# Performance work log

Measured on AMD Instinct MI355X. Metric: run time of the kernel, lower is better.

## Reference

```python
import jax, jax.numpy as jnp
import numpy as np
from jax import lax

K_DIM, E_DIM, H_DIM, BETA = 256, 64, 256, 0.25
DN = ('NCHW', 'OIHW', 'NCHW')


def conv(x, w, b=None, stride=1, pad=0):
    y = lax.conv_general_dilated(x, w, (stride, stride), [(pad, pad), (pad, pad)], dimension_numbers=DN)
    if b is not None:
        y = y + b[None, :, None, None]
    return y


def deconv(x, w, b):
    # torch ConvTranspose2d(k=4, stride=2, pad=1): weight [in, out, kH, kW]
    rhs = jnp.flip(w, (2, 3)).swapaxes(0, 1)  # -> [out, in, kH, kW]
    y = lax.conv_general_dilated(x, rhs, (1, 1), [(2, 2), (2, 2)], lhs_dilation=(2, 2), dimension_numbers=DN)
    return y + b[None, :, None, None]


def res_block(x, w3, w1):
    out = jax.nn.relu(x)
    out = conv(out, w3, stride=1, pad=1)
    out = jax.nn.relu(out)
    out = conv(out, w1, stride=1, pad=0)
    return out + x


def vq_embed(z, codebook):
    # z: [B, C, Hs, Ws]; faithful to original: flatten to (-1, e_dim) even though C != e_dim
    zp = jnp.transpose(z, (0, 2, 3, 1))  # [B,Hs,Ws,C]
    zf = zp.reshape(-1, E_DIM)  # [N, e_dim]
    # ||z||^2 + ||e||^2 - 2 z e^T
    dist = (jnp.sum(zf * zf, axis=1, keepdims=True)
            + jnp.sum(codebook * codebook, axis=1)
            - 2.0 * zf @ codebook.T)  # [N, K]
    idx = jnp.argmin(dist, axis=1)  # [N]
    vq = jnp.take(codebook, idx, axis=0).reshape(zp.shape)  # gather == one-hot matmul
    loss = (jnp.mean((lax.stop_gradient(vq) - zp) ** 2)
            + BETA * jnp.mean((vq - lax.stop_gradient(zp)) ** 2))
    vq_st = zp + lax.stop_gradient(vq - zp)  # straight-through
    return loss, jnp.transpose(vq_st, (0, 3, 1, 2))


def setup_inputs() -> dict:
    key = jax.random.key(0)
    ks = jax.random.split(key, 20)
    f32 = jnp.float32
    s = 0.05
    inp = {
        'x': jax.random.normal(ks[0], (32, 3, 128, 128), f32),
        'enc_w1': jax.random.normal(ks[1], (H_DIM, 3, 4, 4), f32) * s,
        'enc_b1': jnp.zeros((H_DIM,), f32),
        'enc_w2': jax.random.normal(ks[2], (H_DIM, H_DIM, 4, 4), f32) * s,
        'enc_b2': jnp.zeros((H_DIM,), f32),
        'er1_w3': jax.random.normal(ks[3], (H_DIM, H_DIM, 3, 3), f32) * s,
        'er1_w1': jax.random.normal(ks[4], (H_DIM, H_DIM, 1, 1), f32) * s,
        'er2_w3': jax.random.normal(ks[5], (H_DIM, H_DIM, 3, 3), f32) * s,
        'er2_w1': jax.random.normal(ks[6], (H_DIM, H_DIM, 1, 1), f32) * s,
        'codebook': jax.random.uniform(ks[7], (K_DIM, E_DIM), f32, -1.0 / K_DIM, 1.0 / K_DIM),
        'dr1_w3': jax.random.normal(ks[8], (H_DIM, H_DIM, 3, 3), f32) * s,
        'dr1_w1': jax.random.normal(ks[9], (H_DIM, H_DIM, 1, 1), f32) * s,
        'dr2_w3': jax.random.normal(ks[10], (H_DIM, H_DIM, 3, 3), f32) * s,
        'dr2_w1': jax.random.normal(ks[11], (H_DIM, H_DIM, 1, 1), f32) * s,
        'dt1_w': jax.random.normal(ks[12], (H_DIM, H_DIM, 4, 4), f32) * s,  # [in,out,k,k]
        'dt1_b': jnp.zeros((H_DIM,), f32),
        'dt2_w': jax.random.normal(ks[13], (H_DIM, 3, 4, 4), f32) * s,
        'dt2_b': jnp.zeros((3,), f32),
    }
    return inp


def reference(x, enc_w1, enc_b1, enc_w2, enc_b2, er1_w3, er1_w1, er2_w3, er2_w1,
              codebook, dr1_w3, dr1_w1, dr2_w3, dr2_w1, dt1_w, dt1_b, dt2_w, dt2_b):
    # encoder
    z = conv(x, enc_w1, enc_b1, stride=2, pad=1)
    z = conv(z, enc_w2, enc_b2, stride=2, pad=1)
    z = res_block(z, er1_w3, er1_w1)
    z = res_block(z, er2_w3, er2_w1)
    # VQ
    emb_loss, vq_z = vq_embed(z, codebook)
    # decoder
    d = res_block(vq_z, dr1_w3, dr1_w1)
    d = res_block(d, dr2_w3, dr2_w1)
    d = deconv(d, dt1_w, dt1_b)
    d = deconv(d, dt2_w, dt2_b)
    recon = jnp.tanh(d)
    return recon, emb_loss
```

## Files before the change

kernel.cpp:

```cpp
#include <hip/hip_runtime.h>
#include <math.h>


typedef unsigned short ushort;
typedef short bf16x8 __attribute__((ext_vector_type(8)));
typedef float f32x4 __attribute__((ext_vector_type(4)));

__device__ __forceinline__ ushort f2bf(float f) {
    unsigned u = __builtin_bit_cast(unsigned, f);
    unsigned r = (u + 0x7fffu + ((u >> 16) & 1u)) >> 16;
    return (ushort)r;
}
__device__ __forceinline__ float bfl(unsigned u) { return __builtin_bit_cast(float, u << 16); }
__device__ __forceinline__ float bfh(unsigned u) { return __builtin_bit_cast(float, u & 0xffff0000u); }

__device__ __forceinline__ unsigned relu_u(unsigned u) {
    unsigned m = (u >> 15) & 0x00010001u;
    return u & ~((m << 16) - m);
}
__device__ __forceinline__ uint4 relu4(uint4 v) {
    v.x = relu_u(v.x); v.y = relu_u(v.y); v.z = relu_u(v.z); v.w = relu_u(v.w);
    return v;
}

__global__ void k_pack_c3x4(const float* __restrict__ w0, const float* __restrict__ w1,
                            const float* __restrict__ w2, const float* __restrict__ w3,
                            ushort* __restrict__ o0, ushort* __restrict__ o1,
                            ushort* __restrict__ o2, ushort* __restrict__ o3) {
    int layer = blockIdx.x / 2304;
    int i = (blockIdx.x - layer * 2304) * 256 + threadIdx.x;
    const float* w = layer == 0 ? w0 : layer == 1 ? w1 : layer == 2 ? w2 : w3;
    ushort* o = layer == 0 ? o0 : layer == 1 ? o1 : layer == 2 ? o2 : o3;
    int kk = i & 31, co = (i >> 5) & 255, cb = (i >> 13) & 7, t = i >> 16;
    int ci = cb * 32 + kk, kh = t / 3, kw = t % 3;
    o[i] = f2bf(w[((co * 256 + ci) * 3 + kh) * 3 + kw]);
}

__global__ void k_pack_c1x1x4(const float* __restrict__ w0, const float* __restrict__ w1,
                              const float* __restrict__ w2, const float* __restrict__ w3,
                              ushort* __restrict__ o0, ushort* __restrict__ o1,
                              ushort* __restrict__ o2, ushort* __restrict__ o3) {
    int layer = blockIdx.x >> 8;
    int i = (blockIdx.x & 255) * 256 + threadIdx.x;
    const float* w = layer == 0 ? w0 : layer == 1 ? w1 : layer == 2 ? w2 : w3;
    ushort* o = layer == 0 ? o0 : layer == 1 ? o1 : layer == 2 ? o2 : o3;
    int kk = i & 31, co = (i >> 5) & 255, cb = (i >> 13) & 7;
    o[i] = f2bf(w[co * 256 + cb * 32 + kk]);
}

__global__ void k_pack_vq(const float* __restrict__ cb, ushort* __restrict__ apk,
                          float* __restrict__ en) {
    if (blockIdx.x < 64) {
        int i = blockIdx.x * 256 + threadIdx.x;
        int j = i & 7, lane = (i >> 3) & 63, s = (i >> 9) & 1, t = i >> 10;
        int code = t * 16 + (lane & 15);
        int dim = s * 32 + (lane >> 4) * 8 + j;
        apk[i] = f2bf(cb[code * 64 + dim]);
    } else {
        int code = threadIdx.x;
        float s = 0.f;
        for (int d = 0; d < 64; ++d) { float v = cb[code * 64 + d]; s += v * v; }
        en[code] = s;
    }
}

__global__ __launch_bounds__(256) void k_wcomp_enc(const float* __restrict__ w1,
                                                   const float* __restrict__ b1f,
                                                   const float* __restrict__ w2,
                                                   const float* __restrict__ b2f,
                                                   ushort* __restrict__ wenc,
                                                   float* __restrict__ benc,
                                                   float* __restrict__ wct,
                                                   float* __restrict__ wcb,
                                                   float* __restrict__ wcl,
                                                   float* __restrict__ wcr,
                                                   float* __restrict__ wcc) {
    __shared__ float sw1[12288];
    __shared__ float sw2[4096];
    __shared__ float part[2400];
    int co = blockIdx.x, tid = threadIdx.x;
    for (int i = tid; i < 12288; i += 256) sw1[i] = w1[i];
    for (int i = tid; i < 4096; i += 256) sw2[i] = w2[co * 4096 + i];
    __syncthreads();

    {
        float s = 0.f;
#pragma unroll
        for (int t = 0; t < 16; ++t) s += sw2[tid * 16 + t];
        float pb = b1f[tid] * s;
#pragma unroll
        for (int m = 1; m < 64; m <<= 1) pb += __shfl_xor(pb, m);
        if ((tid & 63) == 0) part[tid >> 6] = pb;
    }
    __syncthreads();
    if (tid == 0) benc[co] = b2f[co] + part[0] + part[1] + part[2] + part[3];

    if (tid < 240) {
        int y = tid / 24, rem = tid % 24, ci = rem / 8, ms = rem % 8;
        int na = 0, aa[2], h1[2];
#pragma unroll
        for (int a = 0; a < 4; ++a) {
            int k1 = y - 2 * a;
            if ((unsigned)k1 < 4u) { aa[na] = a; h1[na] = k1; ++na; }
        }
        float acc10[10];
#pragma unroll
        for (int xx = 0; xx < 10; ++xx) acc10[xx] = 0.f;
        for (int m = ms * 32; m < ms * 32 + 32; ++m) {
            for (int pa = 0; pa < na; ++pa) {
                float4 a2 = *(const float4*)&sw2[m * 16 + aa[pa] * 4];
                float4 a1 = *(const float4*)&sw1[m * 48 + ci * 16 + h1[pa] * 4];
                acc10[0] += a2.x * a1.x; acc10[1] += a2.x * a1.y; acc10[2] += a2.x * a1.z; acc10[3] += a2.x * a1.w;
                acc10[2] += a2.y * a1.x; acc10[3] += a2.y * a1.y; acc10[4] += a2.y * a1.z; acc10[5] += a2.y * a1.w;
                acc10[4] += a2.z * a1.x; acc10[5] += a2.z * a1.y; acc10[6] += a2.z * a1.z; acc10[7] += a2.z * a1.w;
                acc10[6] += a2.w * a1.x; acc10[7] += a2.w * a1.y; acc10[8] += a2.w * a1.z; acc10[9] += a2.w * a1.w;
            }
        }
#pragma unroll
        for (int xx = 0; xx < 10; ++xx) part[tid * 10 + xx] = acc10[xx];
    }
    __syncthreads();
    for (int w = tid; w < 320; w += 256) {
        if (w < 300) {
            int y = w / 30, r = w % 30, ci = r / 10, xx = r % 10;
            float s = 0.f;
#pragma unroll
            for (int ms = 0; ms < 8; ++ms) s += part[((y * 24 + ci * 8) + ms) * 10 + xx];
            wenc[(y * 256 + co) * 32 + xx * 3 + ci] = f2bf(s);
        } else {
            int j = w - 300;
            int y = j >> 1;
            wenc[(y * 256 + co) * 32 + 30 + (j & 1)] = 0;
        }
    }

    if (tid < 30 || (tid >= 32 && tid < 62)) {
        bool top = tid < 30;
        int t = top ? tid : tid - 32;
        int xx = t / 3, ci = t % 3;
        int k2hf = top ? 0 : 3, k1hf = top ? 3 : 0;
        float s = 0.f;
        for (int m = 0; m < 256; ++m)
            for (int k2w = 0; k2w < 4; ++k2w) {
                int k1w = xx - 2 * k2w;
                if ((unsigned)k1w < 4u)
                    s += sw2[m * 16 + k2hf * 4 + k2w] * sw1[m * 48 + ci * 16 + k1hf * 4 + k1w];
            }
        (top ? wct : wcb)[t * 256 + co] = s;
    } else if ((tid >= 64 && tid < 94) || (tid >= 96 && tid < 126)) {
        bool left = tid < 94;
        int t = left ? tid - 64 : tid - 96;
        int y = t / 3, ci = t % 3;
        int k2wf = left ? 0 : 3, k1wf = left ? 3 : 0;
        float s = 0.f;
        for (int m = 0; m < 256; ++m)
            for (int k2h = 0; k2h < 4; ++k2h) {
                int k1h = y - 2 * k2h;
                if ((unsigned)k1h < 4u)
                    s += sw2[m * 16 + k2h * 4 + k2wf] * sw1[m * 48 + ci * 16 + k1h * 4 + k1wf];
            }
        (left ? wcl : wcr)[t * 256 + co] = s;
    } else if (tid >= 128 && tid < 140) {
        int c = (tid - 128) / 3, ci = (tid - 128) % 3;
        int k2h = (c >> 1) ? 3 : 0, k2w = (c & 1) ? 3 : 0;
        int k1h = 3 - k2h, k1w = 3 - k2w;
        float s = 0.f;
        for (int m = 0; m < 256; ++m)
            s += sw2[m * 16 + k2h * 4 + k2w] * sw1[m * 48 + ci * 16 + k1h * 4 + k1w];
        wcc[(c * 3 + ci) * 256 + co] = s;
    }
}

__global__ __launch_bounds__(256) void k_wcomp_dec(const float* __restrict__ dt1,
                                                   const float* __restrict__ dt1b,
                                                   const float* __restrict__ dt2,
                                                   const float* __restrict__ dt2b,
                                                   ushort* __restrict__ wdec,
                                                   float* __restrict__ bdec) {
    __shared__ float s1[4096];
    __shared__ float s2[12288];
    __shared__ float part[2400];
    int ci = blockIdx.x, tid = threadIdx.x;
    for (int i = tid; i < 4096; i += 256) s1[i] = dt1[ci * 4096 + i];
    for (int i = tid; i < 12288; i += 256) s2[i] = dt2[i];
    __syncthreads();

    if (ci == 0 && tid < 48) {
        int o = tid >> 4, p = tid & 15, py = p >> 2, px = p & 3;
        int c0 = (py + 1) & 1, d0 = (px + 1) & 1;
        float s = dt2b[o];
        for (int m = 0; m < 256; ++m) {
            float t2 = s2[m * 48 + o * 16 + c0 * 4 + d0] + s2[m * 48 + o * 16 + c0 * 4 + d0 + 2]
                     + s2[m * 48 + o * 16 + (c0 + 2) * 4 + d0] + s2[m * 48 + o * 16 + (c0 + 2) * 4 + d0 + 2];
            s += dt1b[m] * t2;
        }
        bdec[tid] = s;
    }

    if (tid < 240) {
        int y = tid / 24, rem = tid % 24, o = rem / 8, ms = rem % 8;
        int na = 0, aa[2], cc[2];
#pragma unroll
        for (int a = 0; a < 4; ++a) {
            int c = y - 2 * a;
            if ((unsigned)c < 4u) { aa[na] = a; cc[na] = c; ++na; }
        }
        float acc10[10];
#pragma unroll
        for (int xx = 0; xx < 10; ++xx) acc10[xx] = 0.f;
        for (int m = ms * 32; m < ms * 32 + 32; ++m) {
            for (int pa = 0; pa < na; ++pa) {
                float4 d1 = *(const float4*)&s1[m * 16 + aa[pa] * 4];
                float4 d2 = *(const float4*)&s2[m * 48 + o * 16 + cc[pa] * 4];
                acc10[0] += d1.x * d2.x; acc10[1] += d1.x * d2.y; acc10[2] += d1.x * d2.z; acc10[3] += d1.x * d2.w;
                acc10[2] += d1.y * d2.x; acc10[3] += d1.y * d2.y; acc10[4] += d1.y * d2.z; acc10[5] += d1.y * d2.w;
                acc10[4] += d1.z * d2.x; acc10[5] += d1.z * d2.y; acc10[6] += d1.z * d2.z; acc10[7] += d1.z * d2.w;
                acc10[6] += d1.w * d2.x; acc10[7] += d1.w * d2.y; acc10[8] += d1.w * d2.z; acc10[9] += d1.w * d2.w;
            }
        }
#pragma unroll
        for (int xx = 0; xx < 10; ++xx) part[tid * 10 + xx] = acc10[xx];
    }
    __syncthreads();
    for (int w = tid; w < 300; w += 256) {
        int y = w / 30, r = w % 30, o = r / 10, xx = r % 10;
        float s = 0.f;
#pragma unroll
        for (int ms = 0; ms < 8; ++ms) s += part[((y * 24 + o * 8) + ms) * 10 + xx];
        int du = (y < 3) ? 1 : (y < 7) ? 0 : -1;
        int py = y - 3 + 4 * du;
        int dv = (xx < 3) ? 1 : (xx < 7) ? 0 : -1;
        int px = xx - 3 + 4 * dv;
        int t = (du + 1) * 3 + (dv + 1);
        int cb2 = ci >> 5, kk = ci & 31;
        wdec[((((t * 3 + o) * 8 + cb2) * 16 + py * 4 + px) * 32) + kk] = f2bf(s);
    }
}

__global__ void k_xpack(const float* __restrict__ x, ushort* __restrict__ xpk) {
    int i = blockIdx.x * 256 + threadIdx.x;
    int k = i & 31, ow = (i >> 5) & 31, r = (i >> 10) & 127, n = i >> 17;
    float v = 0.f;
    if (k < 30) {
        int ci = k % 3, kw = k / 3;
        int col = 4 * ow - 3 + kw;
        if ((unsigned)col < 128u) v = x[((n * 3 + ci) * 128 + r) * 128 + col];
    }
    xpk[i] = f2bf(v);
}

__global__ __launch_bounds__(128) void k_enc_comp(const ushort* __restrict__ xpk,
                                                  const ushort* __restrict__ wenc,
                                                  const float* __restrict__ benc,
                                                  ushort* __restrict__ obf) {
    int tid = threadIdx.x, lane = tid & 63, wv = tid >> 6;
    int q = lane >> 4, l15 = lane & 15;
    int b = blockIdx.x;
    int mblk = b & 7, coslab = (b >> 3) & 3, n = b >> 5;
    int R0 = mblk * 4 + wv * 2;
    int aoff = (coslab * 64 + l15) * 32 + q * 8;

    f32x4 acc[4][4];
#pragma unroll
    for (int at = 0; at < 4; ++at)
#pragma unroll
        for (int bt = 0; bt < 4; ++bt) acc[at][bt] = 0.f;

    for (int t = 0; t < 10; ++t) {
        bf16x8 af[4];
#pragma unroll
        for (int at = 0; at < 4; ++at)
            af[at] = *(const bf16x8*)(wenc + t * 8192 + aoff + at * 512);
#pragma unroll
        for (int bt2 = 0; bt2 < 2; ++bt2) {
            int irow = 4 * (R0 + bt2) + t - 3;
            if ((unsigned)irow >= 128u) continue;
            bf16x8 bf[2];
#pragma unroll
            for (int hb = 0; hb < 2; ++hb) {
                int ow = hb * 16 + l15;
                bf[hb] = *(const bf16x8*)(xpk + (((long)n * 128 + irow) * 32 + ow) * 32 + q * 8);
            }
#pragma unroll
            for (int at = 0; at < 4; ++at)
#pragma unroll
                for (int hb = 0; hb < 2; ++hb)
                    acc[at][bt2 * 2 + hb] = __builtin_amdgcn_mfma_f32_16x16x32_bf16(
                        af[at], bf[hb], acc[at][bt2 * 2 + hb], 0, 0, 0);
        }
    }

    int co_base = coslab * 64;
#pragma unroll
    for (int at = 0; at < 4; ++at) {
        int co_t = co_base + at * 16 + q * 4;
        float4 b4 = *(const float4*)(benc + co_t);
        float bv[4] = {b4.x, b4.y, b4.z, b4.w};
#pragma unroll
        for (int bt = 0; bt < 4; ++bt) {
            int m = R0 * 32 + bt * 16 + l15;
            long oaddr = ((long)n * 1024 + m) * 256 + co_t;
            float v[4];
#pragma unroll
            for (int r = 0; r < 4; ++r) v[r] = acc[at][bt][r] + bv[r];
            uint2 pk;
            pk.x = (unsigned)f2bf(v[0]) | ((unsigned)f2bf(v[1]) << 16);
            pk.y = (unsigned)f2bf(v[2]) | ((unsigned)f2bf(v[3]) << 16);
            *(uint2*)(obf + oaddr) = pk;
        }
    }
}

__global__ __launch_bounds__(256) void k_fix_border(const float* __restrict__ x,
                                                    const ushort* __restrict__ xpk,
                                                    const float* __restrict__ wct,
                                                    const float* __restrict__ wcb,
                                                    const float* __restrict__ wcl,
                                                    const float* __restrict__ wcr,
                                                    const float* __restrict__ wcc,
                                                    ushort* __restrict__ X0) {
    int b = blockIdx.x;
    int n = b >> 7, job = b & 127;
    if (job >= 124) return;
    int co = threadIdx.x;

    auto dot_tb = [&](const float* __restrict__ w, int row, int qq) -> float {
        const ushort* xr = xpk + (((long)n * 128 + row) * 32 + qq) * 32;
        float s = 0.f;
        for (int k = 0; k < 30; ++k) s += w[k * 256 + co] * bfl((unsigned)xr[k]);
        return s;
    };
    auto dot_lr = [&](const float* __restrict__ w, int p, int colofs) -> float {
        float s = 0.f;
        for (int y = 0; y < 10; ++y) {
            int row = 4 * p - 3 + y;
            if ((unsigned)row >= 128u) continue;
            for (int ci = 0; ci < 3; ++ci)
                s += w[(y * 3 + ci) * 256 + co] * x[((long)(n * 3 + ci) * 128 + row) * 128 + colofs];
        }
        return s;
    };
    auto corner = [&](int c, int row, int colofs) -> float {
        float s = 0.f;
        for (int ci = 0; ci < 3; ++ci)
            s += wcc[(c * 3 + ci) * 256 + co] * x[((long)(n * 3 + ci) * 128 + row) * 128 + colofs];
        return s;
    };

    int m;
    float corr;
    if (job < 32) {
        int qq = job;
        m = qq;
        corr = dot_tb(wct, 0, qq);
        if (qq == 0)  corr += dot_lr(wcl, 0, 0)   - corner(0, 0, 0);
        if (qq == 31) corr += dot_lr(wcr, 0, 127) - corner(1, 0, 127);
    } else if (job < 64) {
        int qq = job - 32;
        m = 992 + qq;
        corr = dot_tb(wcb, 127, qq);
        if (qq == 0)  corr += dot_lr(wcl, 31, 0)   - corner(2, 127, 0);
        if (qq == 31) corr += dot_lr(wcr, 31, 127) - corner(3, 127, 127);
    } else if (job < 94) {
        int p = job - 63;
        m = 32 * p;
        corr = dot_lr(wcl, p, 0);
    } else {
        int p = job - 93;
        m = 32 * p + 31;
        corr = dot_lr(wcr, p, 127);
    }

    ushort* ptr = X0 + ((long)n * 1024 + m) * 256 + co;
    float v = bfl((unsigned)(*ptr));
    *ptr = f2bf(v - corr);
}

__global__ __launch_bounds__(256, 2) void k_resblock(const ushort* __restrict__ xin,
                                                     const ushort* __restrict__ w3pk,
                                                     const ushort* __restrict__ w1pk,
                                                     ushort* __restrict__ obf) {
    constexpr int BUFU = 4 * 4 * 34 * 8;
    __shared__ __align__(16) ushort sX[2 * BUFU];
    __shared__ __align__(16) ushort sEx[64 * 256];

    int tid = threadIdx.x, lane = tid & 63, wv = tid >> 6;
    int q = lane >> 4, l15 = lane & 15;
    int b = blockIdx.x;
    int rp = b & 15, n = b >> 4;
    int R0 = rp * 2;

    if (tid < 64) {
        int bufi = tid >> 5, rq = (tid >> 1) & 15, cc = (tid & 1) ? 33 : 0;
        uint4 z; z.x = z.y = z.z = z.w = 0;
        *(uint4*)&sX[bufi * BUFU + (rq * 34 + cc) * 8] = z;
    }

    int brr[4], bcol[4];
#pragma unroll
    for (int bt = 0; bt < 4; ++bt) {
        int p = bt * 16 + l15;
        brr[bt] = p >> 5; bcol[bt] = (p & 31) + 1;
    }

    int scol = lane >> 1, j0 = (lane & 1) * 2;
    int aoff = (wv * 64 + l15) * 32 + q * 8;

    f32x4 acc[4][4];
#pragma unroll
    for (int at = 0; at < 4; ++at)
#pragma unroll
        for (int bt = 0; bt < 4; ++bt) acc[at][bt] = 0.f;

    int hh = R0 - 1 + wv;
    bool hvalid = (unsigned)hh < 32u;
    uint4 sreg[2];
    auto stage_load = [&](int cb2) {
        long off = (((long)n * 32 + hh) * 32 + scol) * 256 + cb2 * 32 + j0 * 8;
#pragma unroll
        for (int k = 0; k < 2; ++k) {
            uint4 v;
            if (hvalid) v = relu4(*(const uint4*)(xin + off + k * 8));
            else { v.x = 0; v.y = 0; v.z = 0; v.w = 0; }
            sreg[k] = v;
        }
    };
    auto write_stage = [&](int pbuf) {
        ushort* bufp = sX + pbuf * BUFU;
#pragma unroll
        for (int k = 0; k < 2; ++k)
            *(uint4*)&bufp[((wv * 4 + j0 + k) * 34 + scol + 1) * 8] = sreg[k];
    };

    stage_load(0);
    write_stage(0);
    __syncthreads();

    for (int cb = 0; cb < 8; ++cb) {
        ushort* bufp = sX + (cb & 1) * BUFU;
        if (cb + 1 < 8) stage_load(cb + 1);
        const ushort* wb = w3pk + (long)cb * 8192 + aoff;

        bf16x8 afc[4];
#pragma unroll
        for (int at = 0; at < 4; ++at) afc[at] = *(const bf16x8*)(wb + at * 512);
#pragma unroll
        for (int t = 0; t < 9; ++t) {
            bf16x8 afn[4];
            if (t < 8) {
#pragma unroll
                for (int at = 0; at < 4; ++at)
                    afn[at] = *(const bf16x8*)(wb + (long)(t + 1) * 65536 + at * 512);
            }
            int taprow = t / 3, dx = t % 3 - 1;
            bf16x8 bfr[4];
#pragma unroll
            for (int bt = 0; bt < 4; ++bt)
                bfr[bt] = *(const bf16x8*)&bufp[(((brr[bt] + taprow) * 4 + q) * 34 + bcol[bt] + dx) * 8];
#pragma unroll
            for (int at = 0; at < 4; ++at)
#pragma unroll
                for (int bt = 0; bt < 4; ++bt)
                    acc[at][bt] = __builtin_amdgcn_mfma_f32_16x16x32_bf16(afc[at], bfr[bt],
                                                                          acc[at][bt], 0, 0, 0);
            if (t < 8) {
#pragma unroll
                for (int at = 0; at < 4; ++at) afc[at] = afn[at];
            }
        }

        if (cb + 1 < 8) {
            write_stage((cb + 1) & 1);
            __syncthreads();
        }
    }

#pragma unroll
    for (int at = 0; at < 4; ++at) {
        int co_t = wv * 64 + at * 16 + q * 4;
#pragma unroll
        for (int bt = 0; bt < 4; ++bt) {
            int px = bt * 16 + l15;
            uint2 pk;
            pk.x = (unsigned)f2bf(fmaxf(acc[at][bt][0], 0.f))
                 | ((unsigned)f2bf(fmaxf(acc[at][bt][1], 0.f)) << 16);
            pk.y = (unsigned)f2bf(fmaxf(acc[at][bt][2], 0.f))
                 | ((unsigned)f2bf(fmaxf(acc[at][bt][3], 0.f)) << 16);
            *(uint2*)&sEx[px * 256 + (co_t ^ ((px & 7) << 3))] = pk;
        }
    }
    __syncthreads();

    f32x4 acc2[4][4];
#pragma unroll
    for (int at = 0; at < 4; ++at)
#pragma unroll
        for (int bt = 0; bt < 4; ++bt) acc2[at][bt] = 0.f;

    for (int cb = 0; cb < 8; ++cb) {
        const ushort* wb1 = w1pk + (long)cb * 8192 + aoff;
        bf16x8 af1[4];
#pragma unroll
        for (int at = 0; at < 4; ++at) af1[at] = *(const bf16x8*)(wb1 + at * 512);
        bf16x8 bf1[4];
#pragma unroll
        for (int bt = 0; bt < 4; ++bt) {
            int px = bt * 16 + l15;
            bf1[bt] = *(const bf16x8*)&sEx[px * 256 + ((cb * 32 + q * 8) ^ ((px & 7) << 3))];
        }
#pragma unroll
        for (int at = 0; at < 4; ++at)
#pragma unroll
            for (int bt = 0; bt < 4; ++bt)
                acc2[at][bt] = __builtin_amdgcn_mfma_f32_16x16x32_bf16(af1[at], bf1[bt],
                                                                      acc2[at][bt], 0, 0, 0);
    }

#pragma unroll
    for (int at = 0; at < 4; ++at) {
        int co_t = wv * 64 + at * 16 + q * 4;
#pragma unroll
        for (int bt = 0; bt < 4; ++bt) {
            int m = R0 * 32 + bt * 16 + l15;
            long oaddr = ((long)n * 1024 + m) * 256 + co_t;
            uint2 rr = *(const uint2*)(xin + oaddr);
            float v[4];
            v[0] = acc2[at][bt][0] + bfl(rr.x);
            v[1] = acc2[at][bt][1] + bfh(rr.x);
            v[2] = acc2[at][bt][2] + bfl(rr.y);
            v[3] = acc2[at][bt][3] + bfh(rr.y);
            uint2 pk;
            pk.x = (unsigned)f2bf(v[0]) | ((unsigned)f2bf(v[1]) << 16);
            pk.y = (unsigned)f2bf(v[2]) | ((unsigned)f2bf(v[3]) << 16);
            *(uint2*)(obf + oaddr) = pk;
        }
    }
}

__global__ __launch_bounds__(256) void k_vq2(const ushort* __restrict__ zb,
                                             const ushort* __restrict__ apk,
                                             const float* __restrict__ en,
                                             const float* __restrict__ cbf,
                                             ushort* __restrict__ vqb,
                                             float* __restrict__ loss) {
    __shared__ int sIdx[64];
    __shared__ float sLoss[64];
    int tid = threadIdx.x, lane = tid & 63, wv = tid >> 6;
    int q = lane >> 4, l15 = lane & 15;
    int r0 = blockIdx.x * 64;
    int R = r0 + wv * 16;

    const ushort* zp = zb + ((long)(R + l15)) * 64 + q * 8;
    bf16x8 b0 = *(const bf16x8*)zp;
    bf16x8 b1 = *(const bf16x8*)(zp + 32);

    float z2 = 0.f;
    {
        const unsigned* u0 = (const unsigned*)&b0;
        const unsigned* u1 = (const unsigned*)&b1;
#pragma unroll
        for (int i = 0; i < 4; ++i) {
            float a = bfl(u0[i]), bb = bfh(u0[i]);
            float c = bfl(u1[i]), d = bfh(u1[i]);
            z2 += a * a + bb * bb + c * c + d * d;
        }
    }

    float best = 3.4e38f;
    int bidx = 0;
#pragma unroll
    for (int t = 0; t < 16; ++t) {
        bf16x8 a0 = *(const bf16x8*)(apk + ((t * 2 + 0) * 64 + lane) * 8);
        bf16x8 a1 = *(const bf16x8*)(apk + ((t * 2 + 1) * 64 + lane) * 8);
        f32x4 acc = {0.f, 0.f, 0.f, 0.f};
        acc = __builtin_amdgcn_mfma_f32_16x16x32_bf16(a0, b0, acc, 0, 0, 0);
        acc = __builtin_amdgcn_mfma_f32_16x16x32_bf16(a1, b1, acc, 0, 0, 0);
        float4 e4 = *(const float4*)(en + t * 16 + q * 4);
        float sc[4] = {e4.x - 2.f * acc[0], e4.y - 2.f * acc[1],
                       e4.z - 2.f * acc[2], e4.w - 2.f * acc[3]};
#pragma unroll
        for (int r = 0; r < 4; ++r) {
            int code = t * 16 + q * 4 + r;
            if (sc[r] < best) { best = sc[r]; bidx = code; }
        }
    }
#pragma unroll
    for (int m = 16; m <= 32; m <<= 1) {
        float ob = __shfl_xor(best, m);
        int oi = __shfl_xor(bidx, m);
        if (ob < best || (ob == best && oi < bidx)) { best = ob; bidx = oi; }
        z2 += __shfl_xor(z2, m);
    }
    if (q == 0) {
        sIdx[wv * 16 + l15] = bidx;
        sLoss[wv * 16 + l15] = best + z2;
    }
    __syncthreads();

    if (wv == 0) {
        float l = sLoss[lane];
#pragma unroll
        for (int m = 1; m < 64; m <<= 1) l += __shfl_xor(l, m);
        if (lane == 0) atomicAdd(loss, l * (1.25f / 8388608.f));
    }

    unsigned* vb = (unsigned*)(vqb + (long)r0 * 64);
#pragma unroll
    for (int k = 0; k < 8; ++k) {
        int i = k * 256 + tid;
        int rl = i >> 5, jp = i & 31;
        int idx = sIdx[rl];
        float v0 = cbf[idx * 64 + 2 * jp];
        float v1 = cbf[idx * 64 + 2 * jp + 1];
        vb[i] = (unsigned)f2bf(v0) | ((unsigned)f2bf(v1) << 16);
    }
}

__global__ __launch_bounds__(128, 2) void k_dec_comp(const ushort* __restrict__ xin,
                                                     const ushort* __restrict__ wdec,
                                                     const float* __restrict__ bdec,
                                                     float* __restrict__ out) {
    constexpr int BUFU = 3 * 4 * 34 * 8;
    constexpr int WLDS = 2 * BUFU;
    __shared__ __align__(16) ushort sX[2 * WLDS];

    int tid = threadIdx.x, lane = tid & 63, wv = tid >> 6;
    int q = lane >> 4, l15 = lane & 15;
    int b = blockIdx.x;
    int rp = b & 15, n = b >> 4;
    int U = rp * 2 + wv;
    ushort* sW = sX + wv * WLDS;

    if (lane < 48) {
        int cc = (lane & 1) ? 33 : 0;
        int sq = lane >> 1;
        uint4 z; z.x = z.y = z.z = z.w = 0;
        *(uint4*)&sW[(sq * 34 + cc) * 8] = z;
    }
    int scol = lane >> 1, j0 = (lane & 1) * 2;

    f32x4 acc[3][2];
#pragma unroll
    for (int o = 0; o < 3; ++o)
#pragma unroll
        for (int bt = 0; bt < 2; ++bt) acc[o][bt] = 0.f;

    uint4 sreg[3][2];
    auto stage_load = [&](int cb2) {
#pragma unroll
        for (int r = 0; r < 3; ++r) {
            int hh = U - 1 + r;
            bool valid = (unsigned)hh < 32u;
            long off = (((long)n * 32 + hh) * 32 + scol) * 256 + cb2 * 32 + j0 * 8;
#pragma unroll
            for (int k = 0; k < 2; ++k) {
                uint4 v;
                if (valid) v = *(const uint4*)(xin + off + k * 8);
                else { v.x = 0; v.y = 0; v.z = 0; v.w = 0; }
                sreg[r][k] = v;
            }
        }
    };
    auto write_stage = [&](int pbuf) {
        ushort* bufp = sW + pbuf * BUFU;
#pragma unroll
        for (int r = 0; r < 3; ++r)
#pragma unroll
            for (int k = 0; k < 2; ++k)
                *(uint4*)&bufp[((r * 4 + j0 + k) * 34 + scol + 1) * 8] = sreg[r][k];
    };

    stage_load(0);
    write_stage(0);

    for (int cb = 0; cb < 8; ++cb) {
        ushort* bufp = sW + (cb & 1) * BUFU;
        if (cb + 1 < 8) stage_load(cb + 1);
        const ushort* wb = wdec + (long)cb * 512 + l15 * 32 + q * 8;
#pragma unroll
        for (int t = 0; t < 9; ++t) {
            int du = t / 3 - 1, dv = t % 3 - 1;
            bf16x8 bfr[2];
#pragma unroll
            for (int bt = 0; bt < 2; ++bt)
                bfr[bt] = *(const bf16x8*)&bufp[(((du + 1) * 4 + q) * 34 + bt * 16 + l15 + 1 + dv) * 8];
#pragma unroll
            for (int o = 0; o < 3; ++o) {
                bf16x8 af = *(const bf16x8*)(wb + (long)(t * 3 + o) * 4096);
#pragma unroll
                for (int bt = 0; bt < 2; ++bt)
                    acc[o][bt] = __builtin_amdgcn_mfma_f32_16x16x32_bf16(af, bfr[bt], acc[o][bt], 0, 0, 0);
            }
        }
        if (cb + 1 < 8) write_stage((cb + 1) & 1);
    }

#pragma unroll
    for (int o = 0; o < 3; ++o) {
#pragma unroll
        for (int bt = 0; bt < 2; ++bt) {
            int V = bt * 16 + l15;
#pragma unroll
            for (int r = 0; r < 4; ++r) {
                int p = q * 4 + r, py = p >> 2, px = p & 3;
                out[(((long)n * 3 + o) * 128 + 4 * U + py) * 128 + 4 * V + px] =
                    tanhf(acc[o][bt][r] + bdec[o * 16 + p]);
            }
        }
    }
}

extern "C" void kernel_launch(void* const* d_in, const int* in_sizes, int n_in,
                              void* d_out, int out_size, void* d_ws, size_t ws_size,
                              hipStream_t stream) {
    (void)in_sizes; (void)n_in; (void)out_size; (void)ws_size;
    const float* x        = (const float*)d_in[0];
    const float* enc_w1   = (const float*)d_in[1];
    const float* enc_b1   = (const float*)d_in[2];
    const float* enc_w2   = (const float*)d_in[3];
    const float* enc_b2   = (const float*)d_in[4];
    const float* er1_w3   = (const float*)d_in[5];
    const float* er1_w1   = (const float*)d_in[6];
    const float* er2_w3   = (const float*)d_in[7];
    const float* er2_w1   = (const float*)d_in[8];
    const float* codebook = (const float*)d_in[9];
    const float* dr1_w3   = (const float*)d_in[10];
    const float* dr1_w1   = (const float*)d_in[11];
    const float* dr2_w3   = (const float*)d_in[12];
    const float* dr2_w1   = (const float*)d_in[13];
    const float* dt1_w    = (const float*)d_in[14];
    const float* dt1_b    = (const float*)d_in[15];
    const float* dt2_w    = (const float*)d_in[16];
    const float* dt2_b    = (const float*)d_in[17];

    float* recon = (float*)d_out;
    float* loss  = recon + 1572864;

    char* ws = (char*)d_ws;
    size_t off = 0;
    auto alloc = [&](size_t bytes) { char* p = ws + off; off += (bytes + 255) & ~(size_t)255; return p; };
    ushort* X0   = (ushort*)alloc(16777216);
    ushort* X2   = (ushort*)alloc(16777216);
    ushort* X3   = (ushort*)alloc(16777216);
    ushort* X4   = (ushort*)alloc(16777216);
    ushort* xpk  = (ushort*)alloc(8388608);
    ushort* wpk_er13 = (ushort*)alloc(1179648);
    ushort* wpk_er23 = (ushort*)alloc(1179648);
    ushort* wpk_dr13 = (ushort*)alloc(1179648);
    ushort* wpk_dr23 = (ushort*)alloc(1179648);
    ushort* wpk_er11 = (ushort*)alloc(131072);
    ushort* wpk_er21 = (ushort*)alloc(131072);
    ushort* wpk_dr11 = (ushort*)alloc(131072);
    ushort* wpk_dr21 = (ushort*)alloc(131072);
    ushort* wenc     = (ushort*)alloc(163840);
    ushort* wdec     = (ushort*)alloc(221184);
    ushort* apk      = (ushort*)alloc(32768);
    float*  benc     = (float*)alloc(1024);
    float*  bdec     = (float*)alloc(192);
    float*  en       = (float*)alloc(1024);
    float*  wct      = (float*)alloc(32768);
    float*  wcb      = (float*)alloc(32768);
    float*  wcl      = (float*)alloc(32768);
    float*  wcr      = (float*)alloc(32768);
    float*  wcc      = (float*)alloc(12288);

    hipMemsetAsync(loss, 0, sizeof(float), stream);
    hipMemsetAsync(wdec, 0, 221184, stream);

    k_pack_c3x4<<<9216, 256, 0, stream>>>(er1_w3, er2_w3, dr1_w3, dr2_w3,
                                          wpk_er13, wpk_er23, wpk_dr13, wpk_dr23);
    k_pack_c1x1x4<<<1024, 256, 0, stream>>>(er1_w1, er2_w1, dr1_w1, dr2_w1,
                                            wpk_er11, wpk_er21, wpk_dr11, wpk_dr21);
    k_pack_vq<<<65, 256, 0, stream>>>(codebook, apk, en);
    k_wcomp_enc<<<256, 256, 0, stream>>>(enc_w1, enc_b1, enc_w2, enc_b2, wenc, benc,
                                         wct, wcb, wcl, wcr, wcc);
    k_wcomp_dec<<<256, 256, 0, stream>>>(dt1_w, dt1_b, dt2_w, dt2_b, wdec, bdec);
    k_xpack<<<16384, 256, 0, stream>>>(x, xpk);

    k_enc_comp<<<1024, 128, 0, stream>>>(xpk, wenc, benc, X0);
    k_fix_border<<<4096, 256, 0, stream>>>(x, xpk, wct, wcb, wcl, wcr, wcc, X0);
    k_resblock<<<512, 256, 0, stream>>>(X0, wpk_er13, wpk_er11, X2);
    k_resblock<<<512, 256, 0, stream>>>(X2, wpk_er23, wpk_er21, X3);
    k_vq2<<<2048, 256, 0, stream>>>(X3, apk, en, codebook, X4, loss);
    k_resblock<<<512, 256, 0, stream>>>(X4, wpk_dr13, wpk_dr11, X0);
    k_resblock<<<512, 256, 0, stream>>>(X0, wpk_dr23, wpk_dr21, X2);
    k_dec_comp<<<512, 128, 0, stream>>>(X2, wdec, bdec, recon);
}
```

Baseline: 544.9 us.

## Double channel-block staging in resblock and coalesce epilogue stores through LDS

The resblock 3x3 conv now stages two 32-channel blocks per pipeline step, which halves the number of barriers in the main loop. Its shared memory is merged into one union buffer that is reused for the 1x1 stage and for a new fp32 epilogue transpose. Through that transpose the residual add reads and writes full 16-byte rows per pixel instead of scattered 8-byte pieces. The decoder output kernel likewise stages its tanh results in LDS and writes float4-coalesced rows, at the cost of extra barriers and LDS traffic.

```diff
diff --git a/kernel.cpp b/kernel.cpp
--- a/kernel.cpp
+++ b/kernel.cpp
@@ -380,9 +380,9 @@
                                                      const ushort* __restrict__ w3pk,
                                                      const ushort* __restrict__ w1pk,
                                                      ushort* __restrict__ obf) {
-    constexpr int BUFU = 4 * 4 * 34 * 8;
-    __shared__ __align__(16) ushort sX[2 * BUFU];
-    __shared__ __align__(16) ushort sEx[64 * 256];
+    constexpr int BUFU = 16 * 34 * 8;
+    constexpr int BUF2 = 2 * BUFU;
+    __shared__ __align__(16) ushort sAll[2 * BUF2];
 
     int tid = threadIdx.x, lane = tid & 63, wv = tid >> 6;
     int q = lane >> 4, l15 = lane & 15;
@@ -390,10 +390,10 @@
     int rp = b & 15, n = b >> 4;
     int R0 = rp * 2;
 
-    if (tid < 64) {
-        int bufi = tid >> 5, rq = (tid >> 1) & 15, cc = (tid & 1) ? 33 : 0;
+    if (tid < 128) {
+        int bufi = tid >> 6, slot = (tid >> 1) & 31, cc = (tid & 1) ? 33 : 0;
         uint4 z; z.x = z.y = z.z = z.w = 0;
-        *(uint4*)&sX[bufi * BUFU + (rq * 34 + cc) * 8] = z;
+        *(uint4*)&sAll[bufi * BUF2 + (slot * 34 + cc) * 8] = z;
     }
 
     int brr[4], bcol[4];
@@ -414,66 +414,75 @@
 
     int hh = R0 - 1 + wv;
     bool hvalid = (unsigned)hh < 32u;
-    uint4 sreg[2];
-    auto stage_load = [&](int cb2) {
-        long off = (((long)n * 32 + hh) * 32 + scol) * 256 + cb2 * 32 + j0 * 8;
-#pragma unroll
-        for (int k = 0; k < 2; ++k) {
-            uint4 v;
-            if (hvalid) v = relu4(*(const uint4*)(xin + off + k * 8));
-            else { v.x = 0; v.y = 0; v.z = 0; v.w = 0; }
-            sreg[k] = v;
-        }
+    uint4 sreg[4];
+    auto stage_load = [&](int P) {
+        long off0 = (((long)n * 32 + hh) * 32 + scol) * 256 + (2 * P) * 32 + j0 * 8;
+#pragma unroll
+        for (int c = 0; c < 2; ++c)
+#pragma unroll
+            for (int k = 0; k < 2; ++k) {
+                uint4 v;
+                if (hvalid) v = relu4(*(const uint4*)(xin + off0 + c * 32 + k * 8));
+                else { v.x = 0; v.y = 0; v.z = 0; v.w = 0; }
+                sreg[c * 2 + k] = v;
+            }
     };
-    auto write_stage = [&](int pbuf) {
-        ushort* bufp = sX + pbuf * BUFU;
-#pragma unroll
-        for (int k = 0; k < 2; ++k)
-            *(uint4*)&bufp[((wv * 4 + j0 + k) * 34 + scol + 1) * 8] = sreg[k];
+    auto write_stage = [&](int pb) {
+        ushort* bufp = sAll + pb * BUF2;
+#pragma unroll
+        for (int c = 0; c < 2; ++c)
+#pragma unroll
+            for (int k = 0; k < 2; ++k)
+                *(uint4*)&bufp[((c * 16 + wv * 4 + j0 + k) * 34 + scol + 1) * 8] = sreg[c * 2 + k];
     };
 
     stage_load(0);
     write_stage(0);
     __syncthreads();
 
-    for (int cb = 0; cb < 8; ++cb) {
-        ushort* bufp = sX + (cb & 1) * BUFU;
-        if (cb + 1 < 8) stage_load(cb + 1);
-        const ushort* wb = w3pk + (long)cb * 8192 + aoff;
-
-        bf16x8 afc[4];
-#pragma unroll
-        for (int at = 0; at < 4; ++at) afc[at] = *(const bf16x8*)(wb + at * 512);
-#pragma unroll
-        for (int t = 0; t < 9; ++t) {
-            bf16x8 afn[4];
-            if (t < 8) {
+    for (int P = 0; P < 4; ++P) {
+        ushort* bufp = sAll + (P & 1) * BUF2;
+        if (P + 1 < 4) stage_load(P + 1);
+#pragma unroll
+        for (int cbi = 0; cbi < 2; ++cbi) {
+            int cb = 2 * P + cbi;
+            const ushort* wb = w3pk + (long)cb * 8192 + aoff;
+
+            bf16x8 afc[4];
+#pragma unroll
+            for (int at = 0; at < 4; ++at) afc[at] = *(const bf16x8*)(wb + at * 512);
+#pragma unroll
+            for (int t = 0; t < 9; ++t) {
+                bf16x8 afn[4];
+                if (t < 8) {
+#pragma unroll
+                    for (int at = 0; at < 4; ++at)
+                        afn[at] = *(const bf16x8*)(wb + (long)(t + 1) * 65536 + at * 512);
+                }
+                int taprow = t / 3, dx = t % 3 - 1;
+                bf16x8 bfr[4];
+#pragma unroll
+                for (int bt = 0; bt < 4; ++bt)
+                    bfr[bt] = *(const bf16x8*)&bufp[((cbi * 16 + (brr[bt] + taprow) * 4 + q) * 34
+                                                      + bcol[bt] + dx) * 8];
 #pragma unroll
                 for (int at = 0; at < 4; ++at)
-                    afn[at] = *(const bf16x8*)(wb + (long)(t + 1) * 65536 + at * 512);
-            }
-            int taprow = t / 3, dx = t % 3 - 1;
-            bf16x8 bfr[4];
-#pragma unroll
-            for (int bt = 0; bt < 4; ++bt)
-                bfr[bt] = *(const bf16x8*)&bufp[(((brr[bt] + taprow) * 4 + q) * 34 + bcol[bt] + dx) * 8];
-#pragma unroll
-            for (int at = 0; at < 4; ++at)
-#pragma unroll
-                for (int bt = 0; bt < 4; ++bt)
-                    acc[at][bt] = __builtin_amdgcn_mfma_f32_16x16x32_bf16(afc[at], bfr[bt],
-                                                                          acc[at][bt], 0, 0, 0);
-            if (t < 8) {
-#pragma unroll
-                for (int at = 0; at < 4; ++at) afc[at] = afn[at];
-            }
-        }
-
-        if (cb + 1 < 8) {
-            write_stage((cb + 1) & 1);
+#pragma unroll
+                    for (int bt = 0; bt < 4; ++bt)
+                        acc[at][bt] = __builtin_amdgcn_mfma_f32_16x16x32_bf16(afc[at], bfr[bt],
+                                                                              acc[at][bt], 0, 0, 0);
+                if (t < 8) {
+#pragma unroll
+                    for (int at = 0; at < 4; ++at) afc[at] = afn[at];
+                }
+            }
+        }
+        if (P + 1 < 4) {
+            write_stage((P + 1) & 1);
             __syncthreads();
         }
     }
+    __syncthreads();
 
 #pragma unroll
     for (int at = 0; at < 4; ++at) {
@@ -486,7 +495,7 @@
                  | ((unsigned)f2bf(fmaxf(acc[at][bt][1], 0.f)) << 16);
             pk.y = (unsigned)f2bf(fmaxf(acc[at][bt][2], 0.f))
                  | ((unsigned)f2bf(fmaxf(acc[at][bt][3], 0.f)) << 16);
-            *(uint2*)&sEx[px * 256 + (co_t ^ ((px & 7) << 3))] = pk;
+            *(uint2*)&sAll[px * 256 + (co_t ^ ((px & 7) << 3))] = pk;
         }
     }
     __syncthreads();
@@ -506,7 +515,7 @@
 #pragma unroll
         for (int bt = 0; bt < 4; ++bt) {
             int px = bt * 16 + l15;
-            bf1[bt] = *(const bf16x8*)&sEx[px * 256 + ((cb * 32 + q * 8) ^ ((px & 7) << 3))];
+            bf1[bt] = *(const bf16x8*)&sAll[px * 256 + ((cb * 32 + q * 8) ^ ((px & 7) << 3))];
         }
 #pragma unroll
         for (int at = 0; at < 4; ++at)
@@ -516,23 +525,38 @@
                                                                       acc2[at][bt], 0, 0, 0);
     }
 
-#pragma unroll
-    for (int at = 0; at < 4; ++at) {
-        int co_t = wv * 64 + at * 16 + q * 4;
-#pragma unroll
-        for (int bt = 0; bt < 4; ++bt) {
-            int m = R0 * 32 + bt * 16 + l15;
-            long oaddr = ((long)n * 1024 + m) * 256 + co_t;
-            uint2 rr = *(const uint2*)(xin + oaddr);
-            float v[4];
-            v[0] = acc2[at][bt][0] + bfl(rr.x);
-            v[1] = acc2[at][bt][1] + bfh(rr.x);
-            v[2] = acc2[at][bt][2] + bfl(rr.y);
-            v[3] = acc2[at][bt][3] + bfh(rr.y);
-            uint2 pk;
-            pk.x = (unsigned)f2bf(v[0]) | ((unsigned)f2bf(v[1]) << 16);
-            pk.y = (unsigned)f2bf(v[2]) | ((unsigned)f2bf(v[3]) << 16);
-            *(uint2*)(obf + oaddr) = pk;
+    float* ex2 = (float*)sAll;
+#pragma unroll
+    for (int h = 0; h < 2; ++h) {
+        __syncthreads();
+#pragma unroll
+        for (int at = 0; at < 4; ++at) {
+            int co_t = wv * 64 + at * 16 + q * 4;
+#pragma unroll
+            for (int b2 = 0; b2 < 2; ++b2) {
+                int bt = 2 * h + b2;
+                int pxl = bt * 16 + l15 - 32 * h;
+                *(f32x4*)&ex2[pxl * 256 + (co_t ^ ((pxl & 7) << 2))] = acc2[at][bt];
+            }
+        }
+        __syncthreads();
+        int pxl = tid >> 3, cq = (tid & 7) * 32;
+        long gm = (long)n * 1024 + R0 * 32 + 32 * h + pxl;
+        const ushort* rp_ = xin + gm * 256 + cq;
+        ushort* op_ = obf + gm * 256 + cq;
+        int sw = (pxl & 7) << 2;
+#pragma unroll
+        for (int ch = 0; ch < 4; ++ch) {
+            int co0 = cq + ch * 8;
+            uint4 rr = *(const uint4*)(rp_ + ch * 8);
+            float4 e0 = *(float4*)&ex2[pxl * 256 + (co0 ^ sw)];
+            float4 e1 = *(float4*)&ex2[pxl * 256 + ((co0 + 4) ^ sw)];
+            uint4 pk;
+            pk.x = (unsigned)f2bf(e0.x + bfl(rr.x)) | ((unsigned)f2bf(e0.y + bfh(rr.x)) << 16);
+            pk.y = (unsigned)f2bf(e0.z + bfl(rr.y)) | ((unsigned)f2bf(e0.w + bfh(rr.y)) << 16);
+            pk.z = (unsigned)f2bf(e1.x + bfl(rr.z)) | ((unsigned)f2bf(e1.y + bfh(rr.z)) << 16);
+            pk.w = (unsigned)f2bf(e1.z + bfl(rr.w)) | ((unsigned)f2bf(e1.w + bfh(rr.w)) << 16);
+            *(uint4*)(op_ + ch * 8) = pk;
         }
     }
 }
@@ -623,6 +647,7 @@
     constexpr int BUFU = 3 * 4 * 34 * 8;
     constexpr int WLDS = 2 * BUFU;
     __shared__ __align__(16) ushort sX[2 * WLDS];
+    __shared__ __align__(16) float sOut[3072];
 
     int tid = threadIdx.x, lane = tid & 63, wv = tid >> 6;
     int q = lane >> 4, l15 = lane & 15;
@@ -703,10 +728,20 @@
 #pragma unroll
             for (int r = 0; r < 4; ++r) {
                 int p = q * 4 + r, py = p >> 2, px = p & 3;
-                out[(((long)n * 3 + o) * 128 + 4 * U + py) * 128 + 4 * V + px] =
+                sOut[((o * 2 + wv) * 4 + py) * 128 + 4 * V + px] =
                     tanhf(acc[o][bt][r] + bdec[o * 16 + p]);
             }
         }
+    }
+    __syncthreads();
+
+#pragma unroll
+    for (int i = 0; i < 6; ++i) {
+        int idx = i * 128 + tid;
+        int row = idx >> 5, colq = idx & 31;
+        int o = row >> 3, rem = row & 7, wv2 = rem >> 2, py = rem & 3;
+        long g = ((((long)n * 3 + o) * 128) + 4 * (rp * 2 + wv2) + py) * 128 + colq * 4;
+        *(float4*)(out + g) = *(float4*)&sOut[row * 128 + colq * 4];
     }
 }
 
```

New measurement: 584.6 us. 1.07x slower.
